# Optimization experiments

Hardware: AMD Instinct MI355X
Metric: run time of the kernel (lower is better)

Reference implementation:

```python
import jax, jax.numpy as jnp
import numpy as np

D_MODEL = 1024
N_HEADS = 16
HEAD_DIM = D_MODEL // N_HEADS


def setup_inputs() -> dict:
    key = jax.random.key(0)
    k_x, k_wqkv, k_bqkv, k_wp, k_bp = jax.random.split(key, 5)
    B, N = 2, 2048
    x = jax.random.normal(k_x, (B, N, D_MODEL), dtype=jnp.float32)
    s = 1.0 / np.sqrt(D_MODEL)
    w_qkv = jax.random.uniform(k_wqkv, (D_MODEL, 3 * D_MODEL), jnp.float32, -s, s)
    b_qkv = jax.random.uniform(k_bqkv, (3 * D_MODEL,), jnp.float32, -s, s)
    w_proj = jax.random.uniform(k_wp, (D_MODEL, D_MODEL), jnp.float32, -s, s)
    b_proj = jax.random.uniform(k_bp, (D_MODEL,), jnp.float32, -s, s)
    return {"x": x, "w_qkv": w_qkv, "b_qkv": b_qkv, "w_proj": w_proj, "b_proj": b_proj}


def reference(x, w_qkv, b_qkv, w_proj, b_proj):
    B, N, C = x.shape
    scale = HEAD_DIM ** (-0.5)
    qkv = x @ w_qkv + b_qkv  # [B, N, 3C]
    qkv = qkv.reshape(B, N, 3, N_HEADS, HEAD_DIM).transpose(2, 0, 3, 1, 4)
    q, k, v = qkv[0], qkv[1], qkv[2]  # each [B, H, N, Dh]
    p = jnp.einsum('bhnd,bhmd->bhnm', q, k) * scale  # [B, H, N, N]
    p = jax.nn.softmax(p, axis=-1)
    o = jnp.einsum('bhnm,bhmd->bhnd', p, v)  # [B, H, N, Dh]
    o = o.transpose(0, 2, 1, 3).reshape(B, N, C)
    return o @ w_proj + b_proj
```

## Files before the change

kernel.cpp:

```cpp
#include <hip/hip_runtime.h>


typedef short v8s __attribute__((ext_vector_type(8)));
typedef float v4f __attribute__((ext_vector_type(4)));
typedef unsigned int v4u __attribute__((ext_vector_type(4)));

#define QSCALE 0.18033688011112042f

#if defined(__has_builtin)
# if __has_builtin(__builtin_amdgcn_exp2f)
#  define EXP2(x) __builtin_amdgcn_exp2f(x)
# endif
#endif
#ifndef EXP2
static __device__ __forceinline__ float exp2_asm(float x) {
    float r;
    asm volatile("v_exp_f32 %0, %1\n\ts_nop 1" : "=v"(r) : "v"(x));
    return r;
}
# define EXP2(x) exp2_asm(x)
#endif

static __device__ __forceinline__ unsigned short f2bf_fast(float f) {
    union { float f; unsigned int u; } a;
    a.f = f;
    return (unsigned short)((a.u + 0x8000u) >> 16);
}

static __device__ __forceinline__ unsigned int pack_bf16(float lo, float hi) {
    union { float f; unsigned int u; } a, b;
    a.f = lo; b.f = hi;
    return __builtin_amdgcn_perm(b.u + 0x8000u, a.u + 0x8000u, 0x07060302u);
}

#define GLD16(g, l) __builtin_amdgcn_global_load_lds( \
    (const __attribute__((address_space(1))) unsigned int*)(g), \
    (__attribute__((address_space(3))) unsigned int*)(l), 16, 0, 0)

__global__ __launch_bounds__(256) void prep(const float* __restrict__ x,
                                            unsigned short* __restrict__ xb,
                                            const float* __restrict__ w_qkv,
                                            unsigned short* __restrict__ wqkvt,
                                            const float* __restrict__ w_proj,
                                            unsigned short* __restrict__ wprojt) {
    __shared__ float tile[32][33];
    const int bid = blockIdx.x, tid = threadIdx.x;
    if (bid < 4096) {
        int i = bid * 256 + tid;
        float4 f = ((const float4*)x)[i];
        ushort4 o;
        o.x = f2bf_fast(f.x); o.y = f2bf_fast(f.y); o.z = f2bf_fast(f.z); o.w = f2bf_fast(f.w);
        ((ushort4*)xb)[i] = o;
        return;
    }
    const float* w; unsigned short* wt; int R, C, bx, by;
    if (bid < 7168) { w = w_qkv; wt = wqkvt; R = 1024; C = 3072;
                      int t = bid - 4096; bx = t % 96; by = t / 96; }
    else            { w = w_proj; wt = wprojt; R = 1024; C = 1024;
                      int t = bid - 7168; bx = t & 31; by = t >> 5; }
    const int tx = tid & 31, ty = tid >> 5;
    const int c0 = bx * 32, r0 = by * 32;
#pragma unroll
    for (int j = 0; j < 32; j += 8)
        tile[ty + j][tx] = w[(r0 + ty + j) * C + c0 + tx];
    __syncthreads();
#pragma unroll
    for (int j = 0; j < 32; j += 8)
        wt[(c0 + ty + j) * R + r0 + tx] = f2bf_fast(tile[tx][ty + j]);
}

__global__ __launch_bounds__(256) void gemm_bt(const unsigned short* __restrict__ A,
                                               const unsigned short* __restrict__ Bt,
                                               const float* __restrict__ bias,
                                               int M, int N, int K, int mode,
                                               unsigned short* __restrict__ qo,
                                               unsigned short* __restrict__ ko,
                                               unsigned short* __restrict__ vto,
                                               float* __restrict__ outp) {
    __shared__ unsigned short Sh[24576];
    const int tid = threadIdx.x;
    const int wave = tid >> 6, lane = tid & 63;
    const int quad = lane >> 4, l16 = lane & 15;
    const int W = gridDim.x;
    const int id = blockIdx.y * W + blockIdx.x;
    const int s = (id & 7) * (W << 2) + (id >> 3);
    const int bm = (s / W) * 128, bn = (s % W) * 128;
    const int wm = (wave >> 1) * 64, wn = (wave & 1) * 64;
    const int rsw = (quad ^ ((l16 >> 1) & 3)) << 3;

    v4f acc[4][4];
#pragma unroll
    for (int i = 0; i < 4; i++)
#pragma unroll
        for (int j = 0; j < 4; j++) acc[i][j] = (v4f){0.f, 0.f, 0.f, 0.f};

#define GSTAGE(off, kk) do { \
    _Pragma("unroll") \
    for (int i_ = 0; i_ < 2; i_++) { \
        int c_ = i_ * 256 + tid; \
        int r_ = c_ >> 2; \
        int g_ = ((c_ & 3) ^ ((r_ >> 1) & 3)) << 3; \
        GLD16(&A[(bm + r_) * K + (kk) + g_], &Sh[(off) + (c_ << 3)]); \
        GLD16(&Bt[(bn + r_) * K + (kk) + g_], &Sh[(off) + 4096 + (c_ << 3)]); \
    } } while (0)

#define GCOMP(off) do { \
    v8s af_[4], bf_[4]; \
    _Pragma("unroll") \
    for (int mi_ = 0; mi_ < 4; mi_++) \
        af_[mi_] = *(const v8s*)&Sh[(off) + (wm + mi_ * 16 + l16) * 32 + rsw]; \
    _Pragma("unroll") \
    for (int ni_ = 0; ni_ < 4; ni_++) \
        bf_[ni_] = *(const v8s*)&Sh[(off) + 4096 + (wn + ni_ * 16 + l16) * 32 + rsw]; \
    _Pragma("unroll") \
    for (int mi_ = 0; mi_ < 4; mi_++) \
        _Pragma("unroll") \
        for (int ni_ = 0; ni_ < 4; ni_++) \
            acc[mi_][ni_] = __builtin_amdgcn_mfma_f32_16x16x32_bf16( \
                af_[mi_], bf_[ni_], acc[mi_][ni_], 0, 0, 0); \
    } while (0)

    const int nt = K >> 5;
    int o0 = 0, o1 = 8192, o2 = 16384;
    GSTAGE(o0, 0);
    GSTAGE(o1, 32);
    for (int t = 0; t < nt - 1; ++t) {
        asm volatile("s_waitcnt vmcnt(4)" ::: "memory");
        __builtin_amdgcn_s_barrier();
        __builtin_amdgcn_sched_barrier(0);
        if (t + 2 < nt) GSTAGE(o2, (t + 2) << 5);
        GCOMP(o0);
        int tmp = o0; o0 = o1; o1 = o2; o2 = tmp;
    }
    asm volatile("s_waitcnt vmcnt(0)" ::: "memory");
    __builtin_amdgcn_s_barrier();
    __builtin_amdgcn_sched_barrier(0);
    GCOMP(o0);
#undef GSTAGE
#undef GCOMP

    if (mode == 1) {
#pragma unroll
        for (int mi = 0; mi < 4; mi++)
#pragma unroll
            for (int ni = 0; ni < 4; ni++) {
                int col = bn + wn + ni * 16 + l16;
                float bv = bias[col];
                int row0 = bm + wm + mi * 16 + quad * 4;
#pragma unroll
                for (int r = 0; r < 4; r++)
                    outp[(row0 + r) * N + col] = acc[mi][ni][r] + bv;
            }
    } else if (bn < 2048) {
        const int isq = (bn < 1024);
        unsigned short* dst = isq ? qo : ko;
        const float sc = isq ? QSCALE : 1.0f;
        __syncthreads();
#pragma unroll
        for (int mi = 0; mi < 4; mi++)
#pragma unroll
            for (int ni = 0; ni < 4; ni++) {
                int c = wn + ni * 16 + l16;
                float bv = bias[bn + c];
                int r0 = wm + mi * 16 + quad * 4;
#pragma unroll
                for (int r = 0; r < 4; r++)
                    Sh[(r0 + r) * 136 + c] = f2bf_fast((acc[mi][ni][r] + bv) * sc);
            }
        __syncthreads();
        const int bb = bm >> 11, nb = bm & 2047;
#pragma unroll
        for (int j = 0; j < 8; j++) {
            int idx = j * 256 + tid;
            int r = idx >> 4, c8 = idx & 15;
            int rem = (bn + c8 * 8) & 1023;
            int h = rem >> 6, dh = rem & 63;
            *(int4*)&dst[(((bb * 16 + h) << 11) + nb + r) * 64 + dh] =
                *(const int4*)&Sh[r * 136 + c8 * 8];
        }
    } else {
        __syncthreads();
#pragma unroll
        for (int mi = 0; mi < 4; mi++)
#pragma unroll
            for (int ni = 0; ni < 4; ni++) {
                int col = bn + wn + ni * 16 + l16;
                float bv = bias[col];
                ushort4 pk;
                pk.x = f2bf_fast(acc[mi][ni][0] + bv);
                pk.y = f2bf_fast(acc[mi][ni][1] + bv);
                pk.z = f2bf_fast(acc[mi][ni][2] + bv);
                pk.w = f2bf_fast(acc[mi][ni][3] + bv);
                *(ushort4*)&Sh[(wn + ni * 16 + l16) * 136 +
                               wm + ((mi >> 1) * 32) + quad * 8 + ((mi & 1) * 4)] = pk;
            }
        __syncthreads();
        const int b = bm >> 11, n_base = bm & 2047;
#pragma unroll
        for (int j = 0; j < 8; j++) {
            int idx = j * 256 + tid;
            int Lcol = idx >> 4, rc = idx & 15;
            int rem = (bn + Lcol) & 1023;
            int h = rem >> 6, dh = rem & 63;
            *(int4*)&vto[((((b * 16 + h) * 64 + dh) << 11) + n_base + rc * 8)] =
                *(const int4*)&Sh[Lcol * 136 + rc * 8];
        }
    }
}

__global__ __launch_bounds__(256, 2) void attn(const unsigned short* __restrict__ q,
                                               const unsigned short* __restrict__ k,
                                               const unsigned short* __restrict__ vt,
                                               unsigned short* __restrict__ o) {
    __shared__ unsigned short Ks[2][64 * 64];
    __shared__ unsigned short Vs[2][64 * 64];
    const int tid = threadIdx.x;
    const int wave = tid >> 6, lane = tid & 63;
    const int quad = lane >> 4, l16 = lane & 15;
    const int sw = l16 & 7;

    const int id = blockIdx.y * 16 + blockIdx.x;
    const int bh = (id & 7) * 4 + ((id >> 3) & 3);
    const int wq0 = (id >> 5) * 128 + wave * 32;
    const int rowg = bh * 2048 + wq0;

    v8s qf[2][2];
#pragma unroll
    for (int g = 0; g < 2; g++)
#pragma unroll
        for (int half = 0; half < 2; half++)
            qf[g][half] = *(const v8s*)&q[(rowg + g * 16 + l16) * 64 + half * 32 + quad * 8];

    v8s onef;
#pragma unroll
    for (int j = 0; j < 8; j++) onef[j] = (short)0x3F80;

    v4f oacc[2][4];
    v4f lacc[2];
#pragma unroll
    for (int g = 0; g < 2; g++) {
        lacc[g] = (v4f){0.f, 0.f, 0.f, 0.f};
#pragma unroll
        for (int dt = 0; dt < 4; dt++) oacc[g][dt] = (v4f){0.f, 0.f, 0.f, 0.f};
    }

    const unsigned short* kbase = k + (((long)bh << 11) * 64);
    const unsigned short* vbase = vt + (((long)bh * 64) << 11);

#define STAGE(buf, n0s) do { \
    _Pragma("unroll") \
    for (int i_ = 0; i_ < 2; i_++) { \
        int c_ = i_ * 256 + tid; \
        int r_ = c_ >> 3; \
        int chs_ = ((c_ & 7) ^ (r_ & 7)) << 3; \
        GLD16(&kbase[((n0s) + r_) * 64 + chs_], &Ks[buf][c_ << 3]); \
        GLD16(&vbase[(r_ << 11) + (n0s) + chs_], &Vs[buf][c_ << 3]); \
    } } while (0)

    auto tile = [&](const unsigned short* Kc, const unsigned short* Vc) {
        v4f s[2][4];
        __builtin_amdgcn_s_setprio(1);
#pragma unroll
        for (int ni = 0; ni < 4; ni++) {
            int rowk = (ni * 16 + l16) * 64;
            v8s kf0 = *(const v8s*)&Kc[rowk + ((quad ^ sw) << 3)];
            v8s kf1 = *(const v8s*)&Kc[rowk + (((4 + quad) ^ sw) << 3)];
#pragma unroll
            for (int g = 0; g < 2; g++) {
                v4f z = (v4f){0.f, 0.f, 0.f, 0.f};
                z = __builtin_amdgcn_mfma_f32_16x16x32_bf16(kf0, qf[g][0], z, 0, 0, 0);
                z = __builtin_amdgcn_mfma_f32_16x16x32_bf16(kf1, qf[g][1], z, 0, 0, 0);
                s[g][ni] = z;
            }
        }
        __builtin_amdgcn_s_setprio(0);

        v8s af[2][2];
#pragma unroll
        for (int g = 0; g < 2; g++)
#pragma unroll
            for (int t = 0; t < 2; t++) {
                v4u w;
                w[0] = pack_bf16(EXP2(s[g][2 * t][0]),     EXP2(s[g][2 * t][1]));
                w[1] = pack_bf16(EXP2(s[g][2 * t][2]),     EXP2(s[g][2 * t][3]));
                w[2] = pack_bf16(EXP2(s[g][2 * t + 1][0]), EXP2(s[g][2 * t + 1][1]));
                w[3] = pack_bf16(EXP2(s[g][2 * t + 1][2]), EXP2(s[g][2 * t + 1][3]));
                union { v4u u; v8s s8; } cv;
                cv.u = w;
                af[g][t] = cv.s8;
            }

        __builtin_amdgcn_s_setprio(1);
#pragma unroll
        for (int dt = 0; dt < 4; dt++) {
            int rowv = (dt * 16 + l16) * 64;
            v8s vf0 = *(const v8s*)&Vc[rowv + ((quad ^ sw) << 3)];
            v8s vf1 = *(const v8s*)&Vc[rowv + (((4 + quad) ^ sw) << 3)];
#pragma unroll
            for (int g = 0; g < 2; g++) {
                oacc[g][dt] = __builtin_amdgcn_mfma_f32_16x16x32_bf16(af[g][0], vf0, oacc[g][dt], 0, 0, 0);
                oacc[g][dt] = __builtin_amdgcn_mfma_f32_16x16x32_bf16(af[g][1], vf1, oacc[g][dt], 0, 0, 0);
            }
        }
#pragma unroll
        for (int g = 0; g < 2; g++) {
            lacc[g] = __builtin_amdgcn_mfma_f32_16x16x32_bf16(af[g][0], onef, lacc[g], 0, 0, 0);
            lacc[g] = __builtin_amdgcn_mfma_f32_16x16x32_bf16(af[g][1], onef, lacc[g], 0, 0, 0);
        }
        __builtin_amdgcn_s_setprio(0);
    };

    STAGE(0, 0);
    for (int n0 = 0; n0 < 2048; n0 += 128) {
        __syncthreads();
        if (n0 + 64 < 2048) STAGE(1, n0 + 64);
        tile(Ks[0], Vs[0]);
        __syncthreads();
        if (n0 + 128 < 2048) STAGE(0, n0 + 128);
        tile(Ks[1], Vs[1]);
    }
#undef STAGE

    const int b = bh >> 4, h = bh & 15;
#pragma unroll
    for (int g = 0; g < 2; g++)
#pragma unroll
        for (int r = 0; r < 4; r++) {
            float linv = 1.0f / lacc[g][r];
            int n = wq0 + g * 16 + quad * 4 + r;
#pragma unroll
            for (int dt = 0; dt < 4; dt++)
                o[(b * 2048 + n) * 1024 + h * 64 + dt * 16 + l16] =
                    f2bf_fast(oacc[g][dt][r] * linv);
        }
}

extern "C" void kernel_launch(void* const* d_in, const int* in_sizes, int n_in,
                              void* d_out, int out_size, void* d_ws, size_t ws_size,
                              hipStream_t stream) {
    const float* x      = (const float*)d_in[0];
    const float* w_qkv  = (const float*)d_in[1];
    const float* b_qkv  = (const float*)d_in[2];
    const float* w_proj = (const float*)d_in[3];
    const float* b_proj = (const float*)d_in[4];
    float* outp = (float*)d_out;

    unsigned short* ws     = (unsigned short*)d_ws;
    unsigned short* xb     = ws;
    unsigned short* wqkvt  = ws + 4194304;
    unsigned short* wprojt = wqkvt + 3145728;
    unsigned short* qws    = wprojt + 1048576;
    unsigned short* kws    = qws + 4194304;
    unsigned short* vtws   = kws + 4194304;
    unsigned short* ows    = xb;

    prep<<<8192, 256, 0, stream>>>(x, xb, w_qkv, wqkvt, w_proj, wprojt);
    gemm_bt<<<dim3(24, 32), 256, 0, stream>>>(xb, wqkvt, b_qkv, 4096, 3072, 1024, 0,
                                              qws, kws, vtws, nullptr);
    attn<<<dim3(16, 32), 256, 0, stream>>>(qws, kws, vtws, ows);
    gemm_bt<<<dim3(8, 32), 256, 0, stream>>>(ows, wprojt, b_proj, 4096, 1024, 1024, 1,
                                             nullptr, nullptr, nullptr, outp);
}
```

Before: 173.0 us.

## Software-pipeline attention tiles so QK of next tile overlaps exp and PV

Restructures the attention main loop into a two-stage software pipeline. The QK scores for tile i+1 are computed while the exp and PV of tile i run. V is staged into four LDS buffers and K into two, and a combined vmcnt wait plus barrier replaces __syncthreads. The aim is to keep the MFMA units busy across the exp phase and hide global-to-LDS latency, at the cost of more LDS and more registers for two score sets, which could reduce occupancy.

```diff
diff --git a/kernel.cpp b/kernel.cpp
--- a/kernel.cpp
+++ b/kernel.cpp
@@ -212,8 +212,8 @@
                                                const unsigned short* __restrict__ k,
                                                const unsigned short* __restrict__ vt,
                                                unsigned short* __restrict__ o) {
-    __shared__ unsigned short Ks[2][64 * 64];
-    __shared__ unsigned short Vs[2][64 * 64];
+    __shared__ unsigned short KsF[2 * 4096];
+    __shared__ unsigned short VsF[4 * 4096];
     const int tid = threadIdx.x;
     const int wave = tid >> 6, lane = tid & 63;
     const int quad = lane >> 4, l16 = lane & 15;
@@ -247,19 +247,20 @@
     const unsigned short* kbase = k + (((long)bh << 11) * 64);
     const unsigned short* vbase = vt + (((long)bh * 64) << 11);
 
-#define STAGE(buf, n0s) do { \
+#define STAGE(ko, vo, n0s) do { \
     _Pragma("unroll") \
     for (int i_ = 0; i_ < 2; i_++) { \
         int c_ = i_ * 256 + tid; \
         int r_ = c_ >> 3; \
         int chs_ = ((c_ & 7) ^ (r_ & 7)) << 3; \
-        GLD16(&kbase[((n0s) + r_) * 64 + chs_], &Ks[buf][c_ << 3]); \
-        GLD16(&vbase[(r_ << 11) + (n0s) + chs_], &Vs[buf][c_ << 3]); \
+        GLD16(&kbase[((n0s) + r_) * 64 + chs_], &KsF[(ko) + (c_ << 3)]); \
+        GLD16(&vbase[(r_ << 11) + (n0s) + chs_], &VsF[(vo) + (c_ << 3)]); \
     } } while (0)
 
-    auto tile = [&](const unsigned short* Kc, const unsigned short* Vc) {
-        v4f s[2][4];
-        __builtin_amdgcn_s_setprio(1);
+#define WAITB() do { asm volatile("s_waitcnt vmcnt(0)" ::: "memory"); \
+    __builtin_amdgcn_s_barrier(); __builtin_amdgcn_sched_barrier(0); } while (0)
+
+    auto QK = [&](const unsigned short* Kc, v4f (&sreg)[2][4]) {
 #pragma unroll
         for (int ni = 0; ni < 4; ni++) {
             int rowk = (ni * 16 + l16) * 64;
@@ -270,27 +271,26 @@
                 v4f z = (v4f){0.f, 0.f, 0.f, 0.f};
                 z = __builtin_amdgcn_mfma_f32_16x16x32_bf16(kf0, qf[g][0], z, 0, 0, 0);
                 z = __builtin_amdgcn_mfma_f32_16x16x32_bf16(kf1, qf[g][1], z, 0, 0, 0);
-                s[g][ni] = z;
-            }
-        }
-        __builtin_amdgcn_s_setprio(0);
-
-        v8s af[2][2];
+                sreg[g][ni] = z;
+            }
+        }
+    };
+    auto EXPP = [&](v4f (&sreg)[2][4], v8s (&af)[2][2]) {
 #pragma unroll
         for (int g = 0; g < 2; g++)
 #pragma unroll
             for (int t = 0; t < 2; t++) {
                 v4u w;
-                w[0] = pack_bf16(EXP2(s[g][2 * t][0]),     EXP2(s[g][2 * t][1]));
-                w[1] = pack_bf16(EXP2(s[g][2 * t][2]),     EXP2(s[g][2 * t][3]));
-                w[2] = pack_bf16(EXP2(s[g][2 * t + 1][0]), EXP2(s[g][2 * t + 1][1]));
-                w[3] = pack_bf16(EXP2(s[g][2 * t + 1][2]), EXP2(s[g][2 * t + 1][3]));
+                w[0] = pack_bf16(EXP2(sreg[g][2 * t][0]),     EXP2(sreg[g][2 * t][1]));
+                w[1] = pack_bf16(EXP2(sreg[g][2 * t][2]),     EXP2(sreg[g][2 * t][3]));
+                w[2] = pack_bf16(EXP2(sreg[g][2 * t + 1][0]), EXP2(sreg[g][2 * t + 1][1]));
+                w[3] = pack_bf16(EXP2(sreg[g][2 * t + 1][2]), EXP2(sreg[g][2 * t + 1][3]));
                 union { v4u u; v8s s8; } cv;
                 cv.u = w;
                 af[g][t] = cv.s8;
             }
-
-        __builtin_amdgcn_s_setprio(1);
+    };
+    auto PV = [&](v8s (&af)[2][2], const unsigned short* Vc) {
 #pragma unroll
         for (int dt = 0; dt < 4; dt++) {
             int rowv = (dt * 16 + l16) * 64;
@@ -307,19 +307,44 @@
             lacc[g] = __builtin_amdgcn_mfma_f32_16x16x32_bf16(af[g][0], onef, lacc[g], 0, 0, 0);
             lacc[g] = __builtin_amdgcn_mfma_f32_16x16x32_bf16(af[g][1], onef, lacc[g], 0, 0, 0);
         }
+    };
+
+    v4f sA[2][4], sB[2][4];
+    v8s afA[2][2], afB[2][2];
+
+    STAGE(0, 0, 0);
+    WAITB();
+    QK(KsF, sA);
+    STAGE(4096, 4096, 64);
+
+    for (int i = 1; i < 31; i += 2) {
+        WAITB();
+        __builtin_amdgcn_s_setprio(1);
+        EXPP(sA, afA);
+        QK(KsF + 4096, sB);
+        PV(afA, VsF + (((i - 1) & 3) << 12));
         __builtin_amdgcn_s_setprio(0);
-    };
-
-    STAGE(0, 0);
-    for (int n0 = 0; n0 < 2048; n0 += 128) {
-        __syncthreads();
-        if (n0 + 64 < 2048) STAGE(1, n0 + 64);
-        tile(Ks[0], Vs[0]);
-        __syncthreads();
-        if (n0 + 128 < 2048) STAGE(0, n0 + 128);
-        tile(Ks[1], Vs[1]);
-    }
+        STAGE(0, ((i + 1) & 3) << 12, (i + 1) * 64);
+
+        WAITB();
+        __builtin_amdgcn_s_setprio(1);
+        EXPP(sB, afB);
+        QK(KsF, sA);
+        PV(afB, VsF + ((i & 3) << 12));
+        __builtin_amdgcn_s_setprio(0);
+        STAGE(4096, ((i + 2) & 3) << 12, (i + 2) * 64);
+    }
+
+    WAITB();
+    __builtin_amdgcn_s_setprio(1);
+    EXPP(sA, afA);
+    QK(KsF + 4096, sB);
+    PV(afA, VsF + ((30 & 3) << 12));
+    EXPP(sB, afB);
+    PV(afB, VsF + ((31 & 3) << 12));
+    __builtin_amdgcn_s_setprio(0);
 #undef STAGE
+#undef WAITB
 
     const int b = bh >> 4, h = bh & 15;
 #pragma unroll
```

Result: no change. 173.0 us (+0.0%).
